# Kernel optimization log

Measured on AMD Instinct MI355X. Metric: run time of the kernel, lower is better.

## Reference

```python
import jax, jax.numpy as jnp
import numpy as np

H, W, N = 1024, 2048, 1572864
NF, NP, NIN = 32, 3, 5


def _linear_init(key, fan_in, fan_out):
    kw, kb = jax.random.split(key)
    bound = 1.0 / np.sqrt(fan_in)
    w = jax.random.uniform(kw, (fan_in, fan_out), jnp.float32, -bound, bound)
    b = jax.random.uniform(kb, (fan_out,), jnp.float32, -bound, bound)
    return w, b


def setup_inputs() -> dict:
    key = jax.random.key(0)
    ks = jax.random.split(key, 8)
    # grid: sub-pixel source coordinates, (2, N), x-row then y-row
    gx = jax.random.uniform(ks[0], (1, N), jnp.float32) * (W - 1)
    gy = jax.random.uniform(ks[1], (1, N), jnp.float32) * (H - 1)
    grid = jnp.concatenate([gx, gy], axis=0)
    # yi: unique flat pixel indices (torch index-assign assumes no duplicates)
    yi = jax.random.permutation(ks[2], H * W)[:N].astype(jnp.int32)
    # m: near-identity homography so the projective denominator stays well-conditioned
    m = jnp.eye(3, dtype=jnp.float32) + 0.05 * jax.random.normal(ks[3], (3, 3), jnp.float32)
    W1, b1 = _linear_init(ks[4], NIN, NF)
    W2, b2 = _linear_init(ks[5], NF, NF)
    W3, b3 = _linear_init(ks[6], NF, NF)
    W4, b4 = _linear_init(ks[7], NF, NP)
    return {"grid": grid, "yi": yi, "m": m,
            "W1": W1, "b1": b1, "W2": W2, "b2": b2,
            "W3": W3, "b3": b3, "W4": W4, "b4": b4,
            "size_h": H, "size_w": W}


def _calc_dsda_projective(m, h, w):
    # Area scale (Jacobian determinant magnitude) of the homography m at each
    # output pixel: |det(m)| / |m20*x + m21*y + m22|^3, flattened row-major (H*W,)
    xs = jnp.arange(w, dtype=jnp.float32)
    ys = jnp.arange(h, dtype=jnp.float32)
    denom = m[2, 0] * xs[None, :] + m[2, 1] * ys[:, None] + m[2, 2]  # (H, W)
    det = jnp.linalg.det(m)
    return (jnp.abs(det) / (jnp.abs(denom) ** 3)).reshape(-1)


def reference(grid, yi, m, W1, b1, W2, b2, W3, b3, W4, b4, size_h, size_w):
    h, w = size_h, size_w
    # --- feature construction (torch.no_grad block) ---
    dsda = _calc_dsda_projective(m, h, w)[yi][:, None]          # (N, 1) gather
    g = grid.T                                                  # (N, 2)
    gf = jnp.floor(g)
    tl = g - gf                                                 # x-fx, y-fy
    br = 1.0 - tl                                               # fx+1-x, fy+1-y
    x = jax.lax.stop_gradient(jnp.concatenate([tl, br, dsda], axis=1))  # (N, 5)
    # --- tiny 4-layer MLP ---
    hdd = jax.nn.relu(x @ W1 + b1)
    hdd = jax.nn.relu(hdd @ W2 + b2)
    hdd = jax.nn.relu(hdd @ W3 + b3)
    logits = hdd @ W4 + b4                                      # (N, NP)
    wgt = jax.nn.softmax(logits, axis=1)
    # --- scatter back to spatial layout ---
    w_spatial = jnp.zeros((h * w, NP), dtype=wgt.dtype).at[yi].set(wgt)
    return w_spatial.reshape(1, 1, h, w, NP)
```

## Files before the change

### kernel.cpp

```cpp
#include <hip/hip_runtime.h>


#define W_IMG 2048
#define NF    32

typedef __attribute__((ext_vector_type(8))) _Float16 f16x8;
typedef __attribute__((ext_vector_type(4))) _Float16 f16x4;
typedef __attribute__((ext_vector_type(4))) float    f32x4;

__global__ __launch_bounds__(256) void fill_zero(float* __restrict__ out, int n) {
    int n4 = n >> 2;
    float4* o4 = (float4*)out;
    int stride = gridDim.x * blockDim.x;
    for (int i = blockIdx.x * blockDim.x + threadIdx.x; i < n4; i += stride)
        o4[i] = make_float4(0.f, 0.f, 0.f, 0.f);
    int t = (n4 << 2) + (blockIdx.x * blockDim.x + threadIdx.x);
    if (t < n) out[t] = 0.f;
}

__global__ __launch_bounds__(256, 4) void msampler_mlp(
    const float* __restrict__ grid,
    const int*   __restrict__ yi,
    const float* __restrict__ m,
    const float* __restrict__ W1, const float* __restrict__ b1,
    const float* __restrict__ W2, const float* __restrict__ b2,
    const float* __restrict__ W3, const float* __restrict__ b3,
    const float* __restrict__ W4, const float* __restrict__ b4,
    float* __restrict__ out, int N)
{
    const int tid  = threadIdx.x;
    const int lane = tid & 63;
    const int wave = tid >> 6;
    const int lm   = lane & 15;
    const int lq   = lane >> 4;

    __shared__ __align__(16) char smem[4 * 8192];
    char* buf = smem + wave * 8192;

    f16x8 a1[2], a2[2], a3[2], a4;
    f32x4 cb1[2], cb2[2], cb3[2], cb4;
#pragma unroll
    for (int mh = 0; mh < 2; ++mh) {
        int outc = 16 * mh + lm;
#pragma unroll
        for (int j = 0; j < 8; ++j) {
            int k = lq * 8 + j;
            a1[mh][j] = (k < 5) ? (_Float16)W1[k * NF + outc] : (_Float16)0.0f;
            a2[mh][j] = (_Float16)W2[k * NF + outc];
            a3[mh][j] = (_Float16)W3[k * NF + outc];
        }
#pragma unroll
        for (int r = 0; r < 4; ++r) {
            int o = 16 * mh + lq * 4 + r;
            cb1[mh][r] = b1[o];
            cb2[mh][r] = b2[o];
            cb3[mh][r] = b3[o];
        }
    }
#pragma unroll
    for (int j = 0; j < 8; ++j) {
        int k = lq * 8 + j;
        a4[j] = (lm < 3) ? (_Float16)W4[k * 3 + lm] : (_Float16)0.0f;
    }
#pragma unroll
    for (int r = 0; r < 4; ++r) {
        int o = lq * 4 + r;
        cb4[r] = (o < 3) ? b4[o] : 0.f;
    }

    float m00=m[0], m01=m[1], m02=m[2];
    float m10=m[3], m11=m[4], m12=m[5];
    float m20=m[6], m21=m[7], m22=m[8];
    float det = m00*(m11*m22 - m12*m21)
              - m01*(m10*m22 - m12*m20)
              + m02*(m10*m21 - m11*m20);
    float adet = fabsf(det);

    const int i0 = blockIdx.x * 512 + wave * 128;
    int ya[2];
#pragma unroll
    for (int t = 0; t < 2; ++t) {
        int i  = i0 + t * 64 + lane;
        int ic = i < N ? i : N - 1;
        float gx = grid[ic];
        float gy = grid[N + ic];
        int   y  = yi[ic];
        ya[t] = y;
        int py = y >> 11;
        int px = y & (W_IMG - 1);
        float denom = m20*(float)px + m21*(float)py + m22;
        float ad    = fabsf(denom);
        float dsda  = fminf(adet / (ad*ad*ad), 60000.f);
        float fx = gx - floorf(gx);
        float fy = gy - floorf(gy);
        f16x8 f;
        f[0] = (_Float16)fx;         f[1] = (_Float16)fy;
        f[2] = (_Float16)(1.f-fx);   f[3] = (_Float16)(1.f-fy);
        f[4] = (_Float16)dsda;       f[5] = (_Float16)0.0f;
        f[6] = (_Float16)0.0f;       f[7] = (_Float16)0.0f;
        int g = t * 4 + lq;
        *(f16x8*)(buf + g * 1024 + lm * 16) = f;
    }
    {
        f16x8 z = {};
#pragma unroll
        for (int j = 0; j < 6; ++j) {
            int T  = lane >> 3;
            int ch = (lane & 7) + 8 * j;
            *(f16x8*)(buf + T * 1024 + 256 + ch * 16) = z;
        }
    }

    const int woff = ((lq >> 1) * 16 + lm) * 16 + (lq & 1) * 8;

#define LAYER(AF, CB)                                                          \
    _Pragma("unroll")                                                          \
    for (int tg = 0; tg < 2; ++tg) {                                           \
        f16x8 bf[4];                                                           \
        _Pragma("unroll")                                                      \
        for (int q = 0; q < 4; ++q)                                            \
            bf[q] = *(const f16x8*)(buf + (tg*4 + q) * 1024 + lane * 16);      \
        _Pragma("unroll")                                                      \
        for (int q = 0; q < 4; ++q) {                                          \
            int T = tg * 4 + q;                                                \
            _Pragma("unroll")                                                  \
            for (int mh = 0; mh < 2; ++mh) {                                   \
                f32x4 d = __builtin_amdgcn_mfma_f32_16x16x32_f16(              \
                    AF[mh], bf[q], CB[mh], 0, 0, 0);                           \
                f16x4 o;                                                       \
                _Pragma("unroll")                                              \
                for (int r = 0; r < 4; ++r)                                    \
                    o[r] = (_Float16)fminf(fmaxf(d[r], 0.f), 60000.f);         \
                *(f16x4*)(buf + T * 1024 + mh * 512 + woff) = o;               \
            }                                                                  \
        }                                                                      \
    }

    LAYER(a1, cb1)
    LAYER(a2, cb2)
    LAYER(a3, cb3)
#undef LAYER

#pragma unroll
    for (int tg = 0; tg < 2; ++tg) {
        f16x8 bf[4];
#pragma unroll
        for (int q = 0; q < 4; ++q)
            bf[q] = *(const f16x8*)(buf + (tg*4 + q) * 1024 + lane * 16);
#pragma unroll
        for (int q = 0; q < 4; ++q) {
            int T = tg * 4 + q;
            f32x4 d = __builtin_amdgcn_mfma_f32_16x16x32_f16(a4, bf[q], cb4, 0, 0, 0);
            if (lq == 0)
                *(f32x4*)(buf + (T * 16 + lm) * 16) = d;
        }
    }

#pragma unroll
    for (int t = 0; t < 2; ++t) {
        int s = t * 64 + lane;
        f32x4 L = *(const f32x4*)(buf + s * 16);
        float l0 = L[0], l1 = L[1], l2 = L[2];
        float mx = fmaxf(l0, fmaxf(l1, l2));
        float e0 = __expf(l0 - mx), e1 = __expf(l1 - mx), e2 = __expf(l2 - mx);
        float inv = 1.f / (e0 + e1 + e2);
        int i = i0 + s;
        if (i < N) {
            int o = ya[t] * 3;
            out[o + 0] = e0 * inv;
            out[o + 1] = e1 * inv;
            out[o + 2] = e2 * inv;
        }
    }
}

extern "C" void kernel_launch(void* const* d_in, const int* in_sizes, int n_in,
                              void* d_out, int out_size, void* d_ws, size_t ws_size,
                              hipStream_t stream) {
    const float* grid = (const float*)d_in[0];
    const int*   yi   = (const int*)  d_in[1];
    const float* m    = (const float*)d_in[2];
    const float* W1   = (const float*)d_in[3];
    const float* b1   = (const float*)d_in[4];
    const float* W2   = (const float*)d_in[5];
    const float* b2   = (const float*)d_in[6];
    const float* W3   = (const float*)d_in[7];
    const float* b3   = (const float*)d_in[8];
    const float* W4   = (const float*)d_in[9];
    const float* b4   = (const float*)d_in[10];
    float* out = (float*)d_out;

    int N = in_sizes[1];

    fill_zero<<<1024, 256, 0, stream>>>(out, out_size);

    int grid_sz = (N + 511) / 512;
    msampler_mlp<<<grid_sz, 256, 0, stream>>>(
        grid, yi, m, W1, b1, W2, b2, W3, b3, W4, b4, out, N);
}
```

Measured before the change: 128.5 us.

## Scatter packed features into pixel order, run MLP over all pixels densely

```diff
diff --git a/kernel.cpp b/kernel.cpp
--- a/kernel.cpp
+++ b/kernel.cpp
@@ -7,26 +7,53 @@
 typedef __attribute__((ext_vector_type(8))) _Float16 f16x8;
 typedef __attribute__((ext_vector_type(4))) _Float16 f16x4;
 typedef __attribute__((ext_vector_type(4))) float    f32x4;
-
-__global__ __launch_bounds__(256) void fill_zero(float* __restrict__ out, int n) {
-    int n4 = n >> 2;
-    float4* o4 = (float4*)out;
+typedef __attribute__((ext_vector_type(4))) float    fvec4;
+typedef __attribute__((ext_vector_type(4))) int      ivec4;
+
+static __device__ __forceinline__ unsigned packfeat(float fx, float fy) {
+    unsigned short ux = __builtin_bit_cast(unsigned short, (_Float16)fx);
+    unsigned short uy = __builtin_bit_cast(unsigned short, (_Float16)fy);
+    return ((unsigned)uy << 16) | (unsigned)ux;
+}
+
+__global__ __launch_bounds__(256) void scatter_feat(
+    const float* __restrict__ grid, const int* __restrict__ yi,
+    unsigned* __restrict__ feats, int N)
+{
+    int t = blockIdx.x * blockDim.x + threadIdx.x;
     int stride = gridDim.x * blockDim.x;
-    for (int i = blockIdx.x * blockDim.x + threadIdx.x; i < n4; i += stride)
-        o4[i] = make_float4(0.f, 0.f, 0.f, 0.f);
-    int t = (n4 << 2) + (blockIdx.x * blockDim.x + threadIdx.x);
-    if (t < n) out[t] = 0.f;
+    if ((N & 3) == 0) {
+        int n4 = N >> 2;
+        const fvec4* gx4 = (const fvec4*)grid;
+        const fvec4* gy4 = (const fvec4*)(grid + N);
+        const ivec4* yi4 = (const ivec4*)yi;
+        for (int j = t; j < n4; j += stride) {
+            fvec4 x = __builtin_nontemporal_load((fvec4*)(gx4 + j));
+            fvec4 y = __builtin_nontemporal_load((fvec4*)(gy4 + j));
+            ivec4 p = __builtin_nontemporal_load((ivec4*)(yi4 + j));
+#pragma unroll
+            for (int k = 0; k < 4; ++k) {
+                float fx = x[k] - floorf(x[k]);
+                float fy = y[k] - floorf(y[k]);
+                feats[p[k]] = packfeat(fx, fy);
+            }
+        }
+    } else {
+        for (int i = t; i < N; i += stride) {
+            float gx = grid[i], gy = grid[N + i];
+            feats[yi[i]] = packfeat(gx - floorf(gx), gy - floorf(gy));
+        }
+    }
 }
 
 __global__ __launch_bounds__(256, 4) void msampler_mlp(
-    const float* __restrict__ grid,
-    const int*   __restrict__ yi,
+    const unsigned* __restrict__ feats,
     const float* __restrict__ m,
     const float* __restrict__ W1, const float* __restrict__ b1,
     const float* __restrict__ W2, const float* __restrict__ b2,
     const float* __restrict__ W3, const float* __restrict__ b3,
     const float* __restrict__ W4, const float* __restrict__ b4,
-    float* __restrict__ out, int N)
+    float* __restrict__ out, int HW)
 {
     const int tid  = threadIdx.x;
     const int lane = tid & 63;
@@ -77,25 +104,24 @@
     float adet = fabsf(det);
 
     const int i0 = blockIdx.x * 512 + wave * 128;
-    int ya[2];
+    unsigned fwv[2];
 #pragma unroll
     for (int t = 0; t < 2; ++t) {
-        int i  = i0 + t * 64 + lane;
-        int ic = i < N ? i : N - 1;
-        float gx = grid[ic];
-        float gy = grid[N + ic];
-        int   y  = yi[ic];
-        ya[t] = y;
-        int py = y >> 11;
-        int px = y & (W_IMG - 1);
+        int s  = i0 + t * 64 + lane;
+        int sc = s < HW ? s : HW - 1;
+        unsigned w = feats[sc];
+        fwv[t] = w;
+        int py = sc >> 11;
+        int px = sc & (W_IMG - 1);
         float denom = m20*(float)px + m21*(float)py + m22;
         float ad    = fabsf(denom);
         float dsda  = fminf(adet / (ad*ad*ad), 60000.f);
-        float fx = gx - floorf(gx);
-        float fy = gy - floorf(gy);
+        _Float16 hx = __builtin_bit_cast(_Float16, (unsigned short)(w & 0xFFFFu));
+        _Float16 hy = __builtin_bit_cast(_Float16, (unsigned short)(w >> 16));
+        float fxf = (float)hx, fyf = (float)hy;
         f16x8 f;
-        f[0] = (_Float16)fx;         f[1] = (_Float16)fy;
-        f[2] = (_Float16)(1.f-fx);   f[3] = (_Float16)(1.f-fy);
+        f[0] = hx;                   f[1] = hy;
+        f[2] = (_Float16)(1.f-fxf);  f[3] = (_Float16)(1.f-fyf);
         f[4] = (_Float16)dsda;       f[5] = (_Float16)0.0f;
         f[6] = (_Float16)0.0f;       f[7] = (_Float16)0.0f;
         int g = t * 4 + lq;
@@ -164,12 +190,16 @@
         float mx = fmaxf(l0, fmaxf(l1, l2));
         float e0 = __expf(l0 - mx), e1 = __expf(l1 - mx), e2 = __expf(l2 - mx);
         float inv = 1.f / (e0 + e1 + e2);
-        int i = i0 + s;
-        if (i < N) {
-            int o = ya[t] * 3;
-            out[o + 0] = e0 * inv;
-            out[o + 1] = e1 * inv;
-            out[o + 2] = e2 * inv;
+        int gslot = i0 + s;
+        if (gslot < HW) {
+            bool v = (fwv[t] != 0xFFFFFFFFu);
+            float o0 = v ? e0 * inv : 0.f;
+            float o1 = v ? e1 * inv : 0.f;
+            float o2 = v ? e2 * inv : 0.f;
+            int o = gslot * 3;
+            out[o + 0] = o0;
+            out[o + 1] = o1;
+            out[o + 2] = o2;
         }
     }
 }
@@ -190,11 +220,19 @@
     const float* b4   = (const float*)d_in[10];
     float* out = (float*)d_out;
 
-    int N = in_sizes[1];
-
-    fill_zero<<<1024, 256, 0, stream>>>(out, out_size);
-
-    int grid_sz = (N + 511) / 512;
-    msampler_mlp<<<grid_sz, 256, 0, stream>>>(
-        grid, yi, m, W1, b1, W2, b2, W3, b3, W4, b4, out, N);
-}
+    int N  = in_sizes[1];
+    int HW = out_size / 3;
+
+    unsigned* feats = (unsigned*)d_ws;
+
+    hipMemsetAsync(feats, 0xFF, (size_t)HW * sizeof(unsigned), stream);
+
+    int sblocks = ((N >> 2) + 255) / 256;
+    if (sblocks < 1) sblocks = 1;
+    if (sblocks > 4096) sblocks = 4096;
+    scatter_feat<<<sblocks, 256, 0, stream>>>(grid, yi, feats, N);
+
+    int blocks = (HW + 511) / 512;
+    msampler_mlp<<<blocks, 256, 0, stream>>>(
+        feats, m, W1, b1, W2, b2, W3, b3, W4, b4, out, HW);
+}
```

After: 154.8 us. 1.2x slower.

## Scatter packed fp16 softmax pairs to workspace, then expand densely to output

Applied to the files above, without the earlier changes.

```diff
diff --git a/kernel.cpp b/kernel.cpp
--- a/kernel.cpp
+++ b/kernel.cpp
@@ -7,16 +7,6 @@
 typedef __attribute__((ext_vector_type(8))) _Float16 f16x8;
 typedef __attribute__((ext_vector_type(4))) _Float16 f16x4;
 typedef __attribute__((ext_vector_type(4))) float    f32x4;
-
-__global__ __launch_bounds__(256) void fill_zero(float* __restrict__ out, int n) {
-    int n4 = n >> 2;
-    float4* o4 = (float4*)out;
-    int stride = gridDim.x * blockDim.x;
-    for (int i = blockIdx.x * blockDim.x + threadIdx.x; i < n4; i += stride)
-        o4[i] = make_float4(0.f, 0.f, 0.f, 0.f);
-    int t = (n4 << 2) + (blockIdx.x * blockDim.x + threadIdx.x);
-    if (t < n) out[t] = 0.f;
-}
 
 __global__ __launch_bounds__(256, 4) void msampler_mlp(
     const float* __restrict__ grid,
@@ -26,7 +16,7 @@
     const float* __restrict__ W2, const float* __restrict__ b2,
     const float* __restrict__ W3, const float* __restrict__ b3,
     const float* __restrict__ W4, const float* __restrict__ b4,
-    float* __restrict__ out, int N)
+    unsigned* __restrict__ wsp, int N)
 {
     const int tid  = threadIdx.x;
     const int lane = tid & 63;
@@ -90,7 +80,7 @@
         int px = y & (W_IMG - 1);
         float denom = m20*(float)px + m21*(float)py + m22;
         float ad    = fabsf(denom);
-        float dsda  = fminf(adet / (ad*ad*ad), 60000.f);
+        float dsda  = fminf(adet * __builtin_amdgcn_rcpf(ad*ad*ad), 60000.f);
         float fx = gx - floorf(gx);
         float fy = gy - floorf(gy);
         f16x8 f;
@@ -163,14 +153,53 @@
         float l0 = L[0], l1 = L[1], l2 = L[2];
         float mx = fmaxf(l0, fmaxf(l1, l2));
         float e0 = __expf(l0 - mx), e1 = __expf(l1 - mx), e2 = __expf(l2 - mx);
-        float inv = 1.f / (e0 + e1 + e2);
+        float inv = __builtin_amdgcn_rcpf(e0 + e1 + e2);
         int i = i0 + s;
         if (i < N) {
-            int o = ya[t] * 3;
-            out[o + 0] = e0 * inv;
-            out[o + 1] = e1 * inv;
-            out[o + 2] = e2 * inv;
-        }
+            unsigned short u0 =
+                __builtin_bit_cast(unsigned short, (_Float16)(e0 * inv));
+            unsigned short u1 =
+                __builtin_bit_cast(unsigned short, (_Float16)(e1 * inv));
+            wsp[ya[t]] = ((unsigned)u1 << 16) | (unsigned)u0;
+        }
+    }
+}
+
+__global__ __launch_bounds__(256) void expand_out(
+    const unsigned* __restrict__ wsp, float* __restrict__ out, int HW)
+{
+    int t = blockIdx.x * blockDim.x + threadIdx.x;
+    int stride = gridDim.x * blockDim.x;
+    int n4 = HW >> 2;
+    for (int j = t; j < n4; j += stride) {
+        uint4 p = *(const uint4*)(wsp + 4 * j);
+        unsigned pk[4] = {p.x, p.y, p.z, p.w};
+        float w[12];
+#pragma unroll
+        for (int k = 0; k < 4; ++k) {
+            bool v = pk[k] != 0xFFFFFFFFu;
+            float w0 = (float)__builtin_bit_cast(_Float16,
+                           (unsigned short)(pk[k] & 0xFFFFu));
+            float w1 = (float)__builtin_bit_cast(_Float16,
+                           (unsigned short)(pk[k] >> 16));
+            float w2 = fmaxf(1.f - w0 - w1, 0.f);
+            w[3*k + 0] = v ? w0 : 0.f;
+            w[3*k + 1] = v ? w1 : 0.f;
+            w[3*k + 2] = v ? w2 : 0.f;
+        }
+        float4* o = (float4*)(out + (size_t)12 * j);
+        o[0] = make_float4(w[0], w[1],  w[2],  w[3]);
+        o[1] = make_float4(w[4], w[5],  w[6],  w[7]);
+        o[2] = make_float4(w[8], w[9],  w[10], w[11]);
+    }
+    for (int r = (n4 << 2) + t; r < HW; r += stride) {
+        unsigned pk = wsp[r];
+        bool v = pk != 0xFFFFFFFFu;
+        float w0 = (float)__builtin_bit_cast(_Float16, (unsigned short)(pk & 0xFFFFu));
+        float w1 = (float)__builtin_bit_cast(_Float16, (unsigned short)(pk >> 16));
+        out[3*r + 0] = v ? w0 : 0.f;
+        out[3*r + 1] = v ? w1 : 0.f;
+        out[3*r + 2] = v ? fmaxf(1.f - w0 - w1, 0.f) : 0.f;
     }
 }
 
@@ -190,11 +219,18 @@
     const float* b4   = (const float*)d_in[10];
     float* out = (float*)d_out;
 
-    int N = in_sizes[1];
-
-    fill_zero<<<1024, 256, 0, stream>>>(out, out_size);
+    int N  = in_sizes[1];
+    int HW = out_size / 3;
+
+    unsigned* wsp = (unsigned*)d_ws;
+
+    hipMemsetAsync(d_ws, 0xFF, (size_t)HW * sizeof(unsigned), stream);
 
     int grid_sz = (N + 511) / 512;
     msampler_mlp<<<grid_sz, 256, 0, stream>>>(
-        grid, yi, m, W1, b1, W2, b2, W3, b3, W4, b4, out, N);
+        grid, yi, m, W1, b1, W2, b2, W3, b3, W4, b4, wsp, N);
+
+    int eblocks = ((HW >> 2) + 255) / 256;
+    if (eblocks < 1) eblocks = 1;
+    expand_out<<<eblocks, 256, 0, stream>>>(wsp, out, HW);
 }
```

After: 134.6 us. +4.7%, slower.
